# Kernel tuning notes

Hardware: AMD Instinct MI355X
Metric: run time of the kernel (lower is better)

## Reference

```python
import jax, jax.numpy as jnp
import numpy as np

EMB = 512
HID = 512
NCLASS = 50257
BATCH = 64
STEPS = 256


def setup_inputs() -> dict:
    key = jax.random.key(0)
    ks = jax.random.split(key, 14)
    s_e = 1.0 / np.sqrt(EMB)
    s_h = 1.0 / np.sqrt(HID)
    inp = {
        "X": jax.random.randint(ks[0], (BATCH, STEPS), 0, NCLASS, dtype=jnp.int32),
        "emb": jax.random.normal(ks[1], (NCLASS, EMB), jnp.float32) * 0.02,
        # layer 1: gates concatenated in order [i, f, g, o]
        "Wi": jax.random.normal(ks[2], (EMB, 4 * HID), jnp.float32) * s_e,
        "Wh": jax.random.normal(ks[3], (HID, 4 * HID), jnp.float32) * s_h,
        "bi": jax.random.normal(ks[4], (4 * HID,), jnp.float32) * 0.01,
        "bh": jax.random.normal(ks[5], (4 * HID,), jnp.float32) * 0.01,
        # layer 2 (computed but unused for the output, as in the original)
        "Wi1": jax.random.normal(ks[6], (HID, 4 * HID), jnp.float32) * s_h,
        "Wh1": jax.random.normal(ks[7], (HID, 4 * HID), jnp.float32) * s_h,
        "bi1": jax.random.normal(ks[8], (4 * HID,), jnp.float32) * 0.01,
        "bh1": jax.random.normal(ks[9], (4 * HID,), jnp.float32) * 0.01,
        # output projection (nn.Linear(n_hidden, n_class, bias=False) => W: [n_class, n_hidden])
        "Wout": jax.random.normal(ks[10], (NCLASS, HID), jnp.float32) * s_h,
        "bout": jnp.ones((NCLASS,), jnp.float32),
    }
    return inp


def _gates(pre):
    i, f, g, o = jnp.split(pre, 4, axis=-1)
    return jax.nn.sigmoid(i), jax.nn.sigmoid(f), jnp.tanh(g), jax.nn.sigmoid(o)


def reference(X, emb, Wi, Wh, bi, bh, Wi1, Wh1, bi1, bh1, Wout, bout):
    x = emb[X]  # [B, T, E]
    B = x.shape[0]
    # precompute input projections for layer 1 for all timesteps: [T, B, 4H]
    xw = jnp.einsum("bte,eh->tbh", x, Wi) + bi + bh

    h0 = jnp.zeros((B, HID), x.dtype)
    carry0 = (h0, h0, h0, h0)  # h, c, h1, c1

    def step(carry, xw_t):
        h, c, h1, c1 = carry
        i, f, g, o = _gates(xw_t + h @ Wh)
        c = f * c + i * g
        h = o * jnp.tanh(c)
        i1, f1, g1, o1 = _gates(h @ Wi1 + bi1 + h1 @ Wh1 + bh1)
        c1 = f1 * c1 + i1 * g1
        h1 = o1 * jnp.tanh(c1)
        return (h, c, h1, c1), None

    (h, c, h1, c1), _ = jax.lax.scan(step, carry0, xw)
    # original: outputs[-1] is layer-1 h at the last timestep
    return h @ Wout.T + bout
```

## Files before the change

### kernel.cpp

```cpp
#include <hip/hip_runtime.h>
#include <cstdint>
#include <cstddef>

#define EMB    512
#define HID    512
#define NCLASS 50257
#define BATCH  64
#define STEPS  256
#define FOURH  2048
#define HPAD   520

typedef __attribute__((ext_vector_type(8))) short    bf16x8;
typedef __attribute__((ext_vector_type(4))) float    f32x4;
typedef __attribute__((ext_vector_type(2))) _Float16 h2v;
typedef __attribute__((ext_vector_type(8))) _Float16 h8v;

union H8 { h8v v; h2v p[4]; uint4 u; };

__device__ __forceinline__ unsigned short f2bf(float f) {
    union { float f; unsigned int u; } v; v.f = f;
    unsigned int u = v.u;
    return (unsigned short)((u + 0x7fffu + ((u >> 16) & 1u)) >> 16);
}

__device__ __forceinline__ float fdot2f(h2v a, h2v b, float c) {
#if __has_builtin(__builtin_amdgcn_fdot2)
    return __builtin_amdgcn_fdot2(a, b, c, false);
#else
    return fmaf((float)a[0], (float)b[0], fmaf((float)a[1], (float)b[1], c));
#endif
}


__global__ void k_bias(const float* __restrict__ bi, const float* __restrict__ bh,
                       float* __restrict__ bias) {
    int i = blockIdx.x * 256 + threadIdx.x;
    if (i < FOURH) bias[i] = bi[i] + bh[i];
}

__global__ void k_wit(const float* __restrict__ Wi, unsigned short* __restrict__ WiT) {
    int n = blockIdx.x;
    int l = threadIdx.x;
    int k0 = l * 8;
    unsigned short t[8];
#pragma unroll
    for (int i = 0; i < 8; i++)
        t[i] = f2bf(Wi[(size_t)(k0 + i) * FOURH + n]);
    uint4 v;
    v.x = (unsigned)t[0] | ((unsigned)t[1] << 16);
    v.y = (unsigned)t[2] | ((unsigned)t[3] << 16);
    v.z = (unsigned)t[4] | ((unsigned)t[5] << 16);
    v.w = (unsigned)t[6] | ((unsigned)t[7] << 16);
    *(uint4*)(WiT + (size_t)n * EMB + k0) = v;
}

__global__ void k_whT(const float* __restrict__ Wh, _Float16* __restrict__ WhT) {
    int n = blockIdx.x;
    int l = threadIdx.x;
    int j0 = l * 8;
    h8v r;
#pragma unroll
    for (int i = 0; i < 8; i++)
        r[i] = (_Float16)Wh[(size_t)(j0 + i) * FOURH + n];
    *(h8v*)(WhT + (size_t)n * HID + j0) = r;
}

__global__ void k_gather(const int* __restrict__ X, const float* __restrict__ emb,
                         unsigned short* __restrict__ XA) {
    int chunk = blockIdx.x * 256 + threadIdx.x;
    int m  = chunk >> 6;
    int c8 = (chunk & 63) * 8;
    int t = m >> 6, b = m & 63;
    int row = X[b * STEPS + t];
    const float4* src = (const float4*)(emb + (size_t)row * EMB + c8);
    float4 f0 = src[0], f1 = src[1];
    uint4 v;
    v.x = (unsigned)f2bf(f0.x) | ((unsigned)f2bf(f0.y) << 16);
    v.y = (unsigned)f2bf(f0.z) | ((unsigned)f2bf(f0.w) << 16);
    v.z = (unsigned)f2bf(f1.x) | ((unsigned)f2bf(f1.y) << 16);
    v.w = (unsigned)f2bf(f1.z) | ((unsigned)f2bf(f1.w) << 16);
    *(uint4*)(XA + (size_t)m * EMB + c8) = v;
}

__global__ void k_zero(int* __restrict__ p, int n) {
    int i = blockIdx.x * 256 + threadIdx.x;
    if (i < n) p[i] = 0;
}

__global__ __launch_bounds__(256) void k_gemm1(const unsigned short* __restrict__ XA,
                                               const unsigned short* __restrict__ WiT,
                                               const float* __restrict__ bias,
                                               float* __restrict__ XWT) {
    __shared__ unsigned short Al[64 * 48];
    __shared__ unsigned short Bl[64 * 48];
    const int t  = blockIdx.y;
    const int m0 = t * 64;
    const int n0 = blockIdx.x * 64;
    const int tid  = threadIdx.x;
    const int w    = tid >> 6;
    const int lane = tid & 63;
    const int quad = lane >> 4;
    const int l16  = lane & 15;
    const int ar = tid >> 2;
    const int ac = (tid & 3) * 8;

    f32x4 acc[4];
#pragma unroll
    for (int i = 0; i < 4; i++) acc[i] = (f32x4){0.f, 0.f, 0.f, 0.f};

    for (int kk = 0; kk < 16; kk++) {
        const int k0 = kk * 32;
        __syncthreads();
        *(uint4*)(&Al[ar * 48 + ac]) = *(const uint4*)(XA  + (size_t)(m0 + ar) * EMB + k0 + ac);
        *(uint4*)(&Bl[ar * 48 + ac]) = *(const uint4*)(WiT + (size_t)(n0 + ar) * EMB + k0 + ac);
        __syncthreads();
        bf16x8 afrag = *(const bf16x8*)(&Bl[(w * 16 + l16) * 48 + quad * 8]);
#pragma unroll
        for (int mt = 0; mt < 4; mt++) {
            bf16x8 bfrag = *(const bf16x8*)(&Al[(mt * 16 + l16) * 48 + quad * 8]);
            acc[mt] = __builtin_amdgcn_mfma_f32_16x16x32_bf16(afrag, bfrag, acc[mt], 0, 0, 0);
        }
    }
    float bv[4];
#pragma unroll
    for (int r = 0; r < 4; r++) bv[r] = bias[n0 + w * 16 + quad * 4 + r];
#pragma unroll
    for (int mt = 0; mt < 4; mt++)
#pragma unroll
        for (int r = 0; r < 4; r++)
            XWT[((size_t)t * FOURH + n0 + w * 16 + quad * 4 + r) * 64 + mt * 16 + l16]
                = acc[mt][r] + bv[r];
}

__global__ __launch_bounds__(256) void k_step(const float* __restrict__ XWT,
                                              const _Float16* __restrict__ WhT,
                                              _Float16* __restrict__ hG,
                                              float* __restrict__ cG,
                                              float* __restrict__ hfinal,
                                              int t) {
    __shared__ _Float16 WhL[8 * HPAD];
    __shared__ _Float16 hL[76 * HPAD];
    __shared__ float    redL[2 * 8 * 64];

    const int tid = threadIdx.x;
    const int u0  = blockIdx.x * 2;

    const int uq = tid & 1, ub = tid >> 1;
    float xw[4], cold = 0.f;
    if (tid < 128) {
        cold = cG[ub * HID + u0 + uq];
#pragma unroll
        for (int g = 0; g < 4; g++)
            xw[g] = XWT[((size_t)t * FOURH + g * 512 + u0 + uq) * 64 + ub];
    }

#pragma unroll
    for (int it = 0; it < 2; it++) {
        int id = it * 256 + tid;
        int r = id >> 6, off = id & 63;
        int gr = (r >> 1) * 512 + u0 + (r & 1);
        *(uint4*)((char*)WhL + r * (HPAD * 2) + off * 16) =
            *(const uint4*)((const char*)WhT + (size_t)gr * (HID * 2) + off * 16);
    }
    const char* hsrc = (const char*)hG + (size_t)(t & 1) * 65536;
#pragma unroll
    for (int it = 0; it < 16; it++) {
        int id = it * 256 + tid;
        int r = id >> 6, off = id & 63;
        *(uint4*)((char*)hL + r * (HPAD * 2) + off * 16) =
            *(const uint4*)(hsrc + r * 1024 + off * 16);
    }
    __syncthreads();

    const int id7 = tid & 127;
    const int jh  = tid >> 7;
    const int bp  = id7 & 31;
    const int g2  = id7 >> 5;
    const h8v* w0r = (const h8v*)((const char*)WhL + (2 * g2)     * (HPAD * 2)) + jh * 32;
    const h8v* w1r = (const h8v*)((const char*)WhL + (2 * g2 + 1) * (HPAD * 2)) + jh * 32;
    const h8v* h0r = (const h8v*)((const char*)hL  + bp           * (HPAD * 2)) + jh * 32;
    const h8v* h1r = (const h8v*)((const char*)hL  + (bp + 32)    * (HPAD * 2)) + jh * 32;
    float a00 = 0.f, a01 = 0.f, a10 = 0.f, a11 = 0.f;
#pragma unroll 4
    for (int jo = 0; jo < 32; jo++) {
        H8 wv0, wv1, hv0, hv1;
        wv0.v = w0r[jo]; wv1.v = w1r[jo]; hv0.v = h0r[jo]; hv1.v = h1r[jo];
#pragma unroll
        for (int k = 0; k < 4; k++) {
            a00 = fdot2f(hv0.p[k], wv0.p[k], a00);
            a01 = fdot2f(hv1.p[k], wv0.p[k], a01);
            a10 = fdot2f(hv0.p[k], wv1.p[k], a10);
            a11 = fdot2f(hv1.p[k], wv1.p[k], a11);
        }
    }
    redL[jh * 512 + (2 * g2)     * 64 + bp]      = a00;
    redL[jh * 512 + (2 * g2)     * 64 + bp + 32] = a01;
    redL[jh * 512 + (2 * g2 + 1) * 64 + bp]      = a10;
    redL[jh * 512 + (2 * g2 + 1) * 64 + bp + 32] = a11;
    __syncthreads();

    if (tid < 128) {
        float pre[4];
#pragma unroll
        for (int g = 0; g < 4; g++) {
            int cl = 2 * g + uq;
            pre[g] = xw[g] + redL[cl * 64 + ub] + redL[512 + cl * 64 + ub];
        }
        float is = 1.f / (1.f + __expf(-pre[0]));
        float fs = 1.f / (1.f + __expf(-pre[1]));
        float gt = tanhf(pre[2]);
        float os = 1.f / (1.f + __expf(-pre[3]));
        float cnew = fs * cold + is * gt;
        float hnew = os * tanhf(cnew);
        cG[ub * HID + u0 + uq] = cnew;
        hG[(size_t)((t + 1) & 1) * 32768 + ub * HID + u0 + uq] = (_Float16)hnew;
        if (t == STEPS - 1) hfinal[ub * HID + u0 + uq] = hnew;
    }
}

__global__ __launch_bounds__(128) void k_out(const float* __restrict__ Wout,
                                             const float* __restrict__ bout,
                                             const float* __restrict__ hfinal,
                                             float* __restrict__ out) {
    __shared__ float hl[BATCH * 128];
    const int tid = threadIdx.x;
    const int n = blockIdx.x * 128 + tid;
    const bool valid = n < NCLASS;
    float acc[BATCH];
#pragma unroll
    for (int b = 0; b < BATCH; b++) acc[b] = 0.f;
    const float4* W4 = (const float4*)Wout;
    const float4* h4 = (const float4*)hfinal;
    float4* hl4 = (float4*)hl;

    for (int kq = 0; kq < 4; kq++) {
        __syncthreads();
#pragma unroll
        for (int i = 0; i < 16; i++) {
            int f = i * 128 + tid;
            int b = f >> 5, kk = f & 31;
            hl4[f] = h4[b * 128 + kq * 32 + kk];
        }
        __syncthreads();
        if (valid) {
            for (int kk = 0; kk < 32; kk++) {
                float4 wv = W4[(size_t)n * 128 + kq * 32 + kk];
#pragma unroll
                for (int b = 0; b < BATCH; b++) {
                    float4 hv = hl4[b * 32 + kk];
                    acc[b] = fmaf(wv.x, hv.x, acc[b]);
                    acc[b] = fmaf(wv.y, hv.y, acc[b]);
                    acc[b] = fmaf(wv.z, hv.z, acc[b]);
                    acc[b] = fmaf(wv.w, hv.w, acc[b]);
                }
            }
        }
    }
    if (valid) {
        float bv = bout[n];
        for (int b = 0; b < BATCH; b++)
            out[(size_t)b * NCLASS + n] = acc[b] + bv;
    }
}


extern "C" void kernel_launch(void* const* d_in, const int* in_sizes, int n_in,
                              void* d_out, int out_size, void* d_ws, size_t ws_size,
                              hipStream_t stream) {
    const int*   X    = (const int*)  d_in[0];
    const float* emb  = (const float*)d_in[1];
    const float* Wi   = (const float*)d_in[2];
    const float* Wh   = (const float*)d_in[3];
    const float* bi   = (const float*)d_in[4];
    const float* bh   = (const float*)d_in[5];
    const float* Wout = (const float*)d_in[10];
    const float* bout = (const float*)d_in[11];
    float* out = (float*)d_out;

    char* w = (char*)d_ws;
    float*          XWT    = (float*)(w);
    unsigned short* XA     = (unsigned short*)(w + 134217728);
    _Float16*       hG     = (_Float16*)(w + 150732800);
    float*          cG     = (float*)(w + 150863872);
    unsigned short* WiT    = (unsigned short*)(w + 150994944);
    _Float16*       WhT    = (_Float16*)(w + 153092096);
    float*          bias   = (float*)(w + 155189248);
    float*          hfinal = (float*)(w + 155197440);

    k_bias  <<<8,    256, 0, stream>>>(bi, bh, bias);
    k_wit   <<<2048,  64, 0, stream>>>(Wi, WiT);
    k_whT   <<<2048,  64, 0, stream>>>(Wh, WhT);
    k_gather<<<4096, 256, 0, stream>>>(X, emb, XA);
    k_gemm1 <<<dim3(32, 256), 256, 0, stream>>>(XA, WiT, bias, XWT);
    k_zero  <<<256,  256, 0, stream>>>((int*)hG, 65536);
    for (int t = 0; t < STEPS; t++)
        k_step<<<256, 256, 0, stream>>>(XWT, WhT, hG, cG, hfinal, t);
    k_out   <<<393,  128, 0, stream>>>(Wout, bout, hfinal, out);
}
```

Baseline: 1.921 ms.

## Replace per-step LSTM launches with persistent MFMA kernel and flag-based grid sync

Replaces 256 separate k_step launches with a single persistent kernel of 64 blocks. Each block keeps its slice of Wh in registers as f16 MFMA fragments and keeps the cell state in registers. The blocks synchronise each timestep through per-block release/acquire flags in global memory instead of kernel boundaries. Wh is pre-permuted so each block's gate columns are contiguous, and the hidden-state matvec now uses MFMA instead of fdot2. This removes launch overhead and the per-step reload of weights and h. In exchange it depends on all 64 blocks being co-resident, and the spin loop has a guard that can break out early and leave stale h values.

```diff
diff --git a/kernel.cpp b/kernel.cpp
--- a/kernel.cpp
+++ b/kernel.cpp
@@ -8,27 +8,15 @@
 #define BATCH  64
 #define STEPS  256
 #define FOURH  2048
-#define HPAD   520
 
 typedef __attribute__((ext_vector_type(8))) short    bf16x8;
 typedef __attribute__((ext_vector_type(4))) float    f32x4;
-typedef __attribute__((ext_vector_type(2))) _Float16 h2v;
 typedef __attribute__((ext_vector_type(8))) _Float16 h8v;
-
-union H8 { h8v v; h2v p[4]; uint4 u; };
 
 __device__ __forceinline__ unsigned short f2bf(float f) {
     union { float f; unsigned int u; } v; v.f = f;
     unsigned int u = v.u;
     return (unsigned short)((u + 0x7fffu + ((u >> 16) & 1u)) >> 16);
-}
-
-__device__ __forceinline__ float fdot2f(h2v a, h2v b, float c) {
-#if __has_builtin(__builtin_amdgcn_fdot2)
-    return __builtin_amdgcn_fdot2(a, b, c, false);
-#else
-    return fmaf((float)a[0], (float)b[0], fmaf((float)a[1], (float)b[1], c));
-#endif
 }
 
 
@@ -54,15 +42,18 @@
     *(uint4*)(WiT + (size_t)n * EMB + k0) = v;
 }
 
-__global__ void k_whT(const float* __restrict__ Wh, _Float16* __restrict__ WhT) {
-    int n = blockIdx.x;
-    int l = threadIdx.x;
-    int j0 = l * 8;
+__global__ void k_whP(const float* __restrict__ Wh, _Float16* __restrict__ WhP) {
+    int idx = blockIdx.x;
+    int bidb = idx >> 5, c = idx & 31;
+    int ul   = ((c >> 4) << 2) + ((c >> 2) & 3);
+    int gate = c & 3;
+    int gcol = gate * 512 + bidb * 8 + ul;
+    int k0 = threadIdx.x * 8;
     h8v r;
 #pragma unroll
     for (int i = 0; i < 8; i++)
-        r[i] = (_Float16)Wh[(size_t)(j0 + i) * FOURH + n];
-    *(h8v*)(WhT + (size_t)n * HID + j0) = r;
+        r[i] = (_Float16)Wh[(size_t)(k0 + i) * FOURH + gcol];
+    *(h8v*)(WhP + (size_t)idx * 512 + k0) = r;
 }
 
 __global__ void k_gather(const int* __restrict__ X, const float* __restrict__ emb,
@@ -132,89 +123,102 @@
                 = acc[mt][r] + bv[r];
 }
 
-__global__ __launch_bounds__(256) void k_step(const float* __restrict__ XWT,
-                                              const _Float16* __restrict__ WhT,
-                                              _Float16* __restrict__ hG,
-                                              float* __restrict__ cG,
-                                              float* __restrict__ hfinal,
-                                              int t) {
-    __shared__ _Float16 WhL[8 * HPAD];
-    __shared__ _Float16 hL[76 * HPAD];
-    __shared__ float    redL[2 * 8 * 64];
-
-    const int tid = threadIdx.x;
-    const int u0  = blockIdx.x * 2;
-
-    const int uq = tid & 1, ub = tid >> 1;
-    float xw[4], cold = 0.f;
-    if (tid < 128) {
-        cold = cG[ub * HID + u0 + uq];
-#pragma unroll
-        for (int g = 0; g < 4; g++)
-            xw[g] = XWT[((size_t)t * FOURH + g * 512 + u0 + uq) * 64 + ub];
-    }
-
-#pragma unroll
-    for (int it = 0; it < 2; it++) {
-        int id = it * 256 + tid;
-        int r = id >> 6, off = id & 63;
-        int gr = (r >> 1) * 512 + u0 + (r & 1);
-        *(uint4*)((char*)WhL + r * (HPAD * 2) + off * 16) =
-            *(const uint4*)((const char*)WhT + (size_t)gr * (HID * 2) + off * 16);
-    }
-    const char* hsrc = (const char*)hG + (size_t)(t & 1) * 65536;
-#pragma unroll
-    for (int it = 0; it < 16; it++) {
-        int id = it * 256 + tid;
-        int r = id >> 6, off = id & 63;
-        *(uint4*)((char*)hL + r * (HPAD * 2) + off * 16) =
-            *(const uint4*)(hsrc + r * 1024 + off * 16);
-    }
-    __syncthreads();
-
-    const int id7 = tid & 127;
-    const int jh  = tid >> 7;
-    const int bp  = id7 & 31;
-    const int g2  = id7 >> 5;
-    const h8v* w0r = (const h8v*)((const char*)WhL + (2 * g2)     * (HPAD * 2)) + jh * 32;
-    const h8v* w1r = (const h8v*)((const char*)WhL + (2 * g2 + 1) * (HPAD * 2)) + jh * 32;
-    const h8v* h0r = (const h8v*)((const char*)hL  + bp           * (HPAD * 2)) + jh * 32;
-    const h8v* h1r = (const h8v*)((const char*)hL  + (bp + 32)    * (HPAD * 2)) + jh * 32;
-    float a00 = 0.f, a01 = 0.f, a10 = 0.f, a11 = 0.f;
-#pragma unroll 4
-    for (int jo = 0; jo < 32; jo++) {
-        H8 wv0, wv1, hv0, hv1;
-        wv0.v = w0r[jo]; wv1.v = w1r[jo]; hv0.v = h0r[jo]; hv1.v = h1r[jo];
-#pragma unroll
-        for (int k = 0; k < 4; k++) {
-            a00 = fdot2f(hv0.p[k], wv0.p[k], a00);
-            a01 = fdot2f(hv1.p[k], wv0.p[k], a01);
-            a10 = fdot2f(hv0.p[k], wv1.p[k], a10);
-            a11 = fdot2f(hv1.p[k], wv1.p[k], a11);
-        }
-    }
-    redL[jh * 512 + (2 * g2)     * 64 + bp]      = a00;
-    redL[jh * 512 + (2 * g2)     * 64 + bp + 32] = a01;
-    redL[jh * 512 + (2 * g2 + 1) * 64 + bp]      = a10;
-    redL[jh * 512 + (2 * g2 + 1) * 64 + bp + 32] = a11;
-    __syncthreads();
-
-    if (tid < 128) {
-        float pre[4];
-#pragma unroll
-        for (int g = 0; g < 4; g++) {
-            int cl = 2 * g + uq;
-            pre[g] = xw[g] + redL[cl * 64 + ub] + redL[512 + cl * 64 + ub];
-        }
-        float is = 1.f / (1.f + __expf(-pre[0]));
-        float fs = 1.f / (1.f + __expf(-pre[1]));
-        float gt = tanhf(pre[2]);
-        float os = 1.f / (1.f + __expf(-pre[3]));
-        float cnew = fs * cold + is * gt;
-        float hnew = os * tanhf(cnew);
-        cG[ub * HID + u0 + uq] = cnew;
-        hG[(size_t)((t + 1) & 1) * 32768 + ub * HID + u0 + uq] = (_Float16)hnew;
-        if (t == STEPS - 1) hfinal[ub * HID + u0 + uq] = hnew;
+__global__ __launch_bounds__(512, 1) void k_rnn(const float* __restrict__ XWT,
+                                                const _Float16* __restrict__ WhP,
+                                                _Float16* __restrict__ hG,
+                                                float* __restrict__ hfinal,
+                                                unsigned int* __restrict__ flags) {
+    __shared__ _Float16 hw[64 * 8];
+
+    const int tid  = threadIdx.x;
+    const int bid  = blockIdx.x;
+    const int lane = tid & 63;
+    const int wid  = tid >> 6;
+    const int quad = lane >> 4;
+    const int l16  = lane & 15;
+    const int ct   = wid >> 2;
+    const int bt   = wid & 3;
+    const int u    = ct * 4 + quad;
+    const int b    = bt * 16 + l16;
+
+    h8v afrag[16];
+    const _Float16* wsrc = WhP + ((size_t)(bid * 32 + ct * 16 + l16)) * 512 + quad * 8;
+#pragma unroll
+    for (int kk = 0; kk < 16; kk++) afrag[kk] = *(const h8v*)(wsrc + kk * 32);
+
+    float c_state = 0.f;
+    const size_t xwoff = (size_t)(bid * 8 + u) * 64 + b;
+
+    float xw0, xw1, xw2, xw3;
+    {
+        const float* xp = XWT + xwoff;
+        xw0 = xp[0 * 32768]; xw1 = xp[1 * 32768];
+        xw2 = xp[2 * 32768]; xw3 = xp[3 * 32768];
+    }
+
+    for (int t = 0; t < STEPS; t++) {
+        const char* hsrc = (const char*)hG + (size_t)(t & 1) * 65536
+                         + (size_t)b * 1024 + quad * 16;
+
+        f32x4 acc0 = {0.f, 0.f, 0.f, 0.f};
+        f32x4 acc1 = {0.f, 0.f, 0.f, 0.f};
+#pragma unroll
+        for (int kk = 0; kk < 16; kk += 2) {
+            h8v b0 = *(const h8v*)(hsrc + kk * 64);
+            h8v b1 = *(const h8v*)(hsrc + (kk + 1) * 64);
+            acc0 = __builtin_amdgcn_mfma_f32_16x16x32_f16(afrag[kk],     b0, acc0, 0, 0, 0);
+            acc1 = __builtin_amdgcn_mfma_f32_16x16x32_f16(afrag[kk + 1], b1, acc1, 0, 0, 0);
+        }
+        f32x4 acc = acc0 + acc1;
+
+        float pre0 = acc[0] + xw0;
+        float pre1 = acc[1] + xw1;
+        float pre2 = acc[2] + xw2;
+        float pre3 = acc[3] + xw3;
+        float is = 1.f / (1.f + __expf(-pre0));
+        float fs = 1.f / (1.f + __expf(-pre1));
+        float gt = tanhf(pre2);
+        float os = 1.f / (1.f + __expf(-pre3));
+        c_state = fs * c_state + is * gt;
+        float hnew = os * tanhf(c_state);
+
+        if (t == STEPS - 1) {
+            hfinal[(size_t)b * HID + bid * 8 + u] = hnew;
+            break;
+        }
+
+        hw[b * 8 + u] = (_Float16)hnew;
+        __syncthreads();
+        if (tid < 64) {
+            uint4 v = *(const uint4*)(hw + tid * 8);
+            *(uint4*)((char*)hG + (size_t)((t + 1) & 1) * 65536
+                      + (size_t)tid * 1024 + bid * 16) = v;
+            __threadfence();
+        }
+        __syncthreads();
+        if (tid == 0)
+            __hip_atomic_store(&flags[bid * 16], (unsigned)(t + 1),
+                               __ATOMIC_RELEASE, __HIP_MEMORY_SCOPE_AGENT);
+
+        {
+            const float* xp = XWT + (size_t)(t + 1) * FOURH * 64 + xwoff;
+            xw0 = xp[0 * 32768]; xw1 = xp[1 * 32768];
+            xw2 = xp[2 * 32768]; xw3 = xp[3 * 32768];
+        }
+
+        if (tid < 64) {
+            const unsigned tgt = (unsigned)(t + 1);
+            unsigned guard = 0;
+            unsigned v = __hip_atomic_load(&flags[lane * 16],
+                                           __ATOMIC_ACQUIRE, __HIP_MEMORY_SCOPE_AGENT);
+            while (!__all(v >= tgt)) {
+                __builtin_amdgcn_s_sleep(1);
+                if (++guard > (1u << 17)) break;
+                v = __hip_atomic_load(&flags[lane * 16],
+                                      __ATOMIC_ACQUIRE, __HIP_MEMORY_SCOPE_AGENT);
+            }
+        }
+        __syncthreads();
     }
 }
 
@@ -281,19 +285,20 @@
     float*          XWT    = (float*)(w);
     unsigned short* XA     = (unsigned short*)(w + 134217728);
     _Float16*       hG     = (_Float16*)(w + 150732800);
-    float*          cG     = (float*)(w + 150863872);
+    unsigned int*   flags  = (unsigned int*)(w + 150863872);
     unsigned short* WiT    = (unsigned short*)(w + 150994944);
-    _Float16*       WhT    = (_Float16*)(w + 153092096);
+    _Float16*       WhP    = (_Float16*)(w + 153092096);
     float*          bias   = (float*)(w + 155189248);
     float*          hfinal = (float*)(w + 155197440);
 
     k_bias  <<<8,    256, 0, stream>>>(bi, bh, bias);
     k_wit   <<<2048,  64, 0, stream>>>(Wi, WiT);
-    k_whT   <<<2048,  64, 0, stream>>>(Wh, WhT);
+    k_whP   <<<2048,  64, 0, stream>>>(Wh, WhP);
     k_gather<<<4096, 256, 0, stream>>>(X, emb, XA);
     k_gemm1 <<<dim3(32, 256), 256, 0, stream>>>(XA, WiT, bias, XWT);
-    k_zero  <<<256,  256, 0, stream>>>((int*)hG, 65536);
-    for (int t = 0; t < STEPS; t++)
-        k_step<<<256, 256, 0, stream>>>(XWT, WhT, hG, cG, hfinal, t);
+    k_zero  <<<132,  256, 0, stream>>>((int*)hG, 33792);
+
+    k_rnn   <<<64,   512, 0, stream>>>(XWT, WhP, hG, hfinal, flags);
+
     k_out   <<<393,  128, 0, stream>>>(Wout, bout, hfinal, out);
 }
```

Result: slower. 3.002 ms (+56.3%).
